# Kernel optimization log

Measured on AMD Instinct MI355X. Metric: run time of the kernel, lower is better.

Reference implementation:

```python
import jax, jax.numpy as jnp
import numpy as np
from jax import lax

NPOINT = 1024   # number of FPS centroids (init kwarg npoint)
NSAMPLE = 32    # neighbors per group (init kwarg nsample); radius is unused in the source
B, N, D = 8, 4096, 64


def setup_inputs() -> dict:
    key = jax.random.key(0)
    k1, k2, k3 = jax.random.split(key, 3)
    xyz = jax.random.normal(k1, (B, 3, N), dtype=jnp.float32)
    points = jax.random.normal(k2, (B, D, N), dtype=jnp.float32)
    farthest_init = jax.random.randint(k3, (B,), 0, N)
    return {"xyz": xyz, "points": points, "farthest_init": farthest_init}


def _fps(x, farthest_init, npoint):
    # x: [B,N,3] -> centroid indices [B,npoint]. Sequential argmax/min-update, like the torch loop.
    b, n, _ = x.shape
    bidx = jnp.arange(b)

    def step(carry, _):
        dist, far = carry                      # dist: [B,N], far: [B]
        centroid = x[bidx, far]                # [B,3]
        d = jnp.sum((x - centroid[:, None, :]) ** 2, -1)
        dist = jnp.minimum(dist, d)            # == masked update dist[mask]=d[mask]
        return (dist, jnp.argmax(dist, -1)), far

    init = (jnp.full((b, n), 1e10, dtype=x.dtype), farthest_init)
    _, cent = lax.scan(step, init, None, length=npoint)
    return cent.T                              # [B,npoint]


def _forward(xyz, points, farthest_init):
    x = xyz.transpose(0, 2, 1)                 # [B,N,3]
    p = points.transpose(0, 2, 1)              # [B,N,D]
    b = x.shape[0]
    bidx = jnp.arange(b)

    # FPS indices are non-differentiable (long tensor in torch) -> stop_gradient
    fps_idx = _fps(lax.stop_gradient(x), farthest_init, NPOINT)   # [B,S]
    new_xyz = x[bidx[:, None], fps_idx]        # [B,S,3]

    # pairwise squared distances [B,S,N] (same expansion as square_distance)
    sq = (jnp.sum(new_xyz ** 2, -1)[:, :, None]
          + jnp.sum(x ** 2, -1)[:, None, :]
          - 2.0 * jnp.einsum('bsc,bnc->bsn', new_xyz, x))
    # source sorts and takes first nsample == nsample smallest distances
    _, idx = lax.top_k(-lax.stop_gradient(sq), NSAMPLE)           # [B,S,K]

    g_xyz = x[bidx[:, None, None], idx]        # [B,S,K,3]
    g_pts = p[bidx[:, None, None], idx]        # [B,S,K,D]
    new_points = jnp.concatenate([g_xyz, g_pts], -1)              # [B,S,K,3+D]

    # permute(0,3,2,1) then max over dim 2 == max over K then transpose
    feat = jnp.max(new_points, axis=2).transpose(0, 2, 1)         # [B,3+D,S]
    return new_xyz.transpose(0, 2, 1), feat                       # [B,3,S], [B,3+D,S]


def reference(xyz, points, farthest_init):
    return _forward(xyz, points, farthest_init)
```

## Files before the change

kernel.cpp:

```cpp
#include <hip/hip_runtime.h>

#define BB 8
#define NN 4096
#define DD 64
#define SS 1024
#define KK 32
#define GINF 1e30f

typedef float f32x2 __attribute__((ext_vector_type(2)));

__device__ __forceinline__ float fmulrn(float a, float b){ return __fmul_rn(a,b); }
__device__ __forceinline__ float faddrn(float a, float b){ return __fadd_rn(a,b); }
__device__ __forceinline__ float fsubrn(float a, float b){ return __fsub_rn(a,b); }

__device__ __forceinline__ f32x2 pk_add(f32x2 a, f32x2 b){
  f32x2 d; asm("v_pk_add_f32 %0, %1, %2" : "=v"(d) : "v"(a), "v"(b)); return d;
}
__device__ __forceinline__ f32x2 pk_mul(f32x2 a, f32x2 b){
  f32x2 d; asm("v_pk_mul_f32 %0, %1, %2" : "=v"(d) : "v"(a), "v"(b)); return d;
}

template<int CTRL>
__device__ __forceinline__ float dpp_fmax(float v){
  int o = __builtin_amdgcn_update_dpp(0, __float_as_int(v), CTRL, 0xf, 0xf, true);
  return fmaxf(v, __int_as_float(o));
}

__device__ __forceinline__ float fneg_exact(float c){
  return __int_as_float(__float_as_int(c) ^ 0x80000000);
}

__global__ __launch_bounds__(256) void sqx_kernel(const float* __restrict__ xyz,
                                                  float* __restrict__ sqx){
  int i = blockIdx.x * 256 + threadIdx.x;
  int b = i >> 12, n = i & (NN - 1);
  const float* xb = xyz + b * 3 * NN;
  float x = xb[n], y = xb[NN + n], z = xb[2 * NN + n];
  sqx[i] = faddrn(faddrn(fmulrn(x, x), fmulrn(y, y)), fmulrn(z, z));
}

__global__ __launch_bounds__(256) void fps_kernel(const float* __restrict__ xyz,
                                                  const int* __restrict__ finit,
                                                  int* __restrict__ fps_idx){
  __shared__ float4 sc[2][4];
  __shared__ int    sn[2][4];
  int b = blockIdx.x, tid = threadIdx.x;
  int lane = tid & 63, w = tid >> 6;
  const float* xb = xyz + b * 3 * NN;
  f32x2 px2[8], py2[8], pz2[8], dist2[8];
  int nbase = tid << 4;
  #pragma unroll
  for (int p = 0; p < 8; ++p){
    px2[p] = ((const f32x2*)(xb + nbase))[p];
    py2[p] = ((const f32x2*)(xb + NN + nbase))[p];
    pz2[p] = ((const f32x2*)(xb + 2 * NN + nbase))[p];
    dist2[p] = (f32x2){1e10f, 1e10f};
  }
  int far = finit[b];
  float cx = xb[far], cy = xb[NN + far], cz = xb[2 * NN + far];
  if (tid == 0) fps_idx[b * SS] = far;

  for (int it = 0; it < SS - 1; ++it){
    f32x2 c2x = (f32x2){fneg_exact(cx), fneg_exact(cx)};
    f32x2 c2y = (f32x2){fneg_exact(cy), fneg_exact(cy)};
    f32x2 c2z = (f32x2){fneg_exact(cz), fneg_exact(cz)};
    float lmx = 0.0f, lmy = 0.0f;
    #pragma unroll
    for (int p = 0; p < 8; ++p){
      f32x2 tx = pk_add(px2[p], c2x);
      f32x2 ty = pk_add(py2[p], c2y);
      f32x2 tz = pk_add(pz2[p], c2z);
      f32x2 d2 = pk_add(pk_add(pk_mul(tx, tx), pk_mul(ty, ty)), pk_mul(tz, tz));
      dist2[p].x = fminf(dist2[p].x, d2.x);
      dist2[p].y = fminf(dist2[p].y, d2.y);
      lmx = fmaxf(lmx, dist2[p].x);
      lmy = fmaxf(lmy, dist2[p].y);
    }
    float lm = fmaxf(lmx, lmy);
    float v = lm;
    v = dpp_fmax<0x111>(v);
    v = dpp_fmax<0x112>(v);
    v = dpp_fmax<0x114>(v);
    v = dpp_fmax<0x118>(v);
    v = dpp_fmax<0x142>(v);
    v = dpp_fmax<0x143>(v);
    float maxv = __int_as_float(__builtin_amdgcn_readlane(__float_as_int(v), 63));
    int locA = -1, locB = -1;
    float axv = 0.f, ayv = 0.f, azv = 0.f, bxv = 0.f, byv = 0.f, bzv = 0.f;
    #pragma unroll
    for (int j = 15; j >= 8; --j){
      int p = j >> 1;
      float dv = (j & 1) ? dist2[p].y : dist2[p].x;
      if (dv == maxv){
        locB = j;
        bxv = (j & 1) ? px2[p].y : px2[p].x;
        byv = (j & 1) ? py2[p].y : py2[p].x;
        bzv = (j & 1) ? pz2[p].y : pz2[p].x;
      }
    }
    #pragma unroll
    for (int j = 7; j >= 0; --j){
      int p = j >> 1;
      float dv = (j & 1) ? dist2[p].y : dist2[p].x;
      if (dv == maxv){
        locA = j;
        axv = (j & 1) ? px2[p].y : px2[p].x;
        ayv = (j & 1) ? py2[p].y : py2[p].x;
        azv = (j & 1) ? pz2[p].y : pz2[p].x;
      }
    }
    bool fa = locA >= 0;
    int   loc = fa ? locA : locB;
    float scx = fa ? axv : bxv;
    float scy = fa ? ayv : byv;
    float scz = fa ? azv : bzv;
    unsigned long long bal = __ballot(loc >= 0);
    int fl = __ffsll(bal) - 1;
    int par = it & 1;
    if (lane == fl){
      sc[par][w] = make_float4(scx, scy, scz, maxv);
      sn[par][w] = nbase + loc;
    }
    __syncthreads();
    float4 s0 = sc[par][0]; int n0 = sn[par][0];
    #pragma unroll
    for (int q = 1; q < 4; ++q){
      float4 sq_ = sc[par][q]; int nq = sn[par][q];
      if (sq_.w > s0.w){ s0 = sq_; n0 = nq; }
    }
    cx = s0.x; cy = s0.y; cz = s0.z;
    if (tid == 0) fps_idx[b * SS + it + 1] = n0;
  }
}

__global__ __launch_bounds__(256) void knn_kernel(const float* __restrict__ xyz,
                                                  const float* __restrict__ points,
                                                  const float* __restrict__ sqx,
                                                  const int* __restrict__ fps_idx,
                                                  float* __restrict__ out){
  __shared__ int nbr[4][KK];
  int tid = threadIdx.x;
  int lane = tid & 63, wslot = tid >> 6;
  int gw = blockIdx.x * 4 + wslot;
  int b = gw >> 10, cs = gw & 1023;
  const float* xb = xyz + b * 3 * NN;
  const float* sb = sqx + b * NN;
  int c0 = fps_idx[b * SS + cs];
  float cx = xb[c0], cy = xb[NN + c0], cz = xb[2 * NN + c0];
  float sqc = sb[c0];

  float d[64];
  #pragma unroll
  for (int k = 0; k < 64; ++k){
    int n = (k << 6) | lane;
    float xn = xb[n], yn = xb[NN + n], zn = xb[2 * NN + n], sn = sb[n];
    float dot = faddrn(faddrn(fmulrn(cx, xn), fmulrn(cy, yn)), fmulrn(cz, zn));
    d[k] = fsubrn(faddrn(sqc, sn), fmulrn(2.0f, dot));
  }

  float gv[8]; int gn[8];
  #pragma unroll
  for (int j = 0; j < 8; ++j){
    float nv = GINF; int nn2 = 0x40000000;
    #pragma unroll
    for (int t = 0; t < 8; ++t){
      int k = j * 8 + t; int n = (k << 6) | lane;
      if (d[k] < nv){ nv = d[k]; nn2 = n; }
    }
    gv[j] = nv; gn[j] = nn2;
  }

  float lv = -GINF; int ln = -1;
  for (int r = 0; r < KK; ++r){
    float bv = gv[0]; int bn = gn[0];
    #pragma unroll
    for (int j = 1; j < 8; ++j){ if (gv[j] < bv){ bv = gv[j]; bn = gn[j]; } }
    #pragma unroll
    for (int m = 1; m < 64; m <<= 1){
      float ov = __shfl_xor(bv, m);
      int   on = __shfl_xor(bn, m);
      if (ov < bv || (ov == bv && on < bn)){ bv = ov; bn = on; }
    }
    if (lane == 0) nbr[wslot][r] = bn;
    lv = bv; ln = bn;
    int jsel = __builtin_amdgcn_readfirstlane(bn >> 9);
    #define RECOMP(J) if (jsel == (J)) { float nv = GINF; int nn2 = 0x40000000; \
      _Pragma("unroll") \
      for (int t = 0; t < 8; ++t){ int k = (J) * 8 + t; int n = (k << 6) | lane; \
        bool pass = (d[k] > lv) || (d[k] == lv && n > ln); \
        if (pass && d[k] < nv){ nv = d[k]; nn2 = n; } } \
      gv[(J)] = nv; gn[(J)] = nn2; }
    RECOMP(0) RECOMP(1) RECOMP(2) RECOMP(3)
    RECOMP(4) RECOMP(5) RECOMP(6) RECOMP(7)
    #undef RECOMP
  }
  __syncthreads();

  const float* pb = points + b * DD * NN;
  float fm = -GINF, xm = -GINF, ym = -GINF, zm = -GINF;
  #pragma unroll 8
  for (int j = 0; j < KK; ++j){
    int nj = nbr[wslot][j];
    fm = fmaxf(fm, pb[lane * NN + nj]);
    xm = fmaxf(xm, xb[nj]);
    ym = fmaxf(ym, xb[NN + nj]);
    zm = fmaxf(zm, xb[2 * NN + nj]);
  }
  float* out1 = out + BB * 3 * SS;
  float* o1b  = out1 + b * 67 * SS;
  o1b[(3 + lane) * SS + cs] = fm;
  if (lane == 0){
    o1b[cs] = xm; o1b[SS + cs] = ym; o1b[2 * SS + cs] = zm;
    float* o0b = out + b * 3 * SS;
    o0b[cs] = cx; o0b[SS + cs] = cy; o0b[2 * SS + cs] = cz;
  }
}

extern "C" void kernel_launch(void* const* d_in, const int* in_sizes, int n_in,
                              void* d_out, int out_size, void* d_ws, size_t ws_size,
                              hipStream_t stream){
  const float* xyz    = (const float*)d_in[0];
  const float* points = (const float*)d_in[1];
  const int*   finit  = (const int*)d_in[2];
  float* out = (float*)d_out;
  int*   fps_idx = (int*)d_ws;
  float* sqx     = (float*)((char*)d_ws + BB * SS * sizeof(int));

  hipLaunchKernelGGL(sqx_kernel, dim3(BB * NN / 256), dim3(256), 0, stream, xyz, sqx);
  hipLaunchKernelGGL(fps_kernel, dim3(BB), dim3(256), 0, stream, xyz, finit, fps_idx);
  hipLaunchKernelGGL(knn_kernel, dim3(BB * SS / 4), dim3(256), 0, stream,
                     xyz, points, sqx, fps_idx, out);
}
```

Before: 1.258 ms.

## Process two batches per FPS block to interleave independent reduction chains

The FPS kernel now handles two batch elements per 256-thread block and interleaves their distance updates, argmax searches, wave reductions and barriers. The aim is to hide the latency of the serial per-iteration reduction and barrier chain by giving each wave two independent dependency chains, and to halve the barrier count per batch. The local argmax location search now runs before the wave reduction, compared against the lane-local max instead of the wave max. The cost is doubled register use per thread and only four blocks instead of eight, so the work is spread over fewer CUs.

```diff
diff --git a/kernel.cpp b/kernel.cpp
--- a/kernel.cpp
+++ b/kernel.cpp
@@ -24,6 +24,17 @@
 __device__ __forceinline__ float dpp_fmax(float v){
   int o = __builtin_amdgcn_update_dpp(0, __float_as_int(v), CTRL, 0xf, 0xf, true);
   return fmaxf(v, __int_as_float(o));
+}
+
+__device__ __forceinline__ float wave_max_dpp(float lm){
+  float v = lm;
+  v = dpp_fmax<0x111>(v);
+  v = dpp_fmax<0x112>(v);
+  v = dpp_fmax<0x114>(v);
+  v = dpp_fmax<0x118>(v);
+  v = dpp_fmax<0x142>(v);
+  v = dpp_fmax<0x143>(v);
+  return __int_as_float(__builtin_amdgcn_readlane(__float_as_int(v), 63));
 }
 
 __device__ __forceinline__ float fneg_exact(float c){
@@ -42,94 +53,142 @@
 __global__ __launch_bounds__(256) void fps_kernel(const float* __restrict__ xyz,
                                                   const int* __restrict__ finit,
                                                   int* __restrict__ fps_idx){
-  __shared__ float4 sc[2][4];
-  __shared__ int    sn[2][4];
-  int b = blockIdx.x, tid = threadIdx.x;
+  __shared__ float4 scA[2][4], scB[2][4];
+  __shared__ int    snA[2][4], snB[2][4];
+  int blk = blockIdx.x, tid = threadIdx.x;
   int lane = tid & 63, w = tid >> 6;
-  const float* xb = xyz + b * 3 * NN;
-  f32x2 px2[8], py2[8], pz2[8], dist2[8];
+  int bA = blk * 2, bB = blk * 2 + 1;
+  const float* xA = xyz + bA * 3 * NN;
+  const float* xB = xyz + bB * 3 * NN;
   int nbase = tid << 4;
+
+  f32x2 pxA[8], pyA[8], pzA[8], ddA[8];
+  f32x2 pxB[8], pyB[8], pzB[8], ddB[8];
   #pragma unroll
   for (int p = 0; p < 8; ++p){
-    px2[p] = ((const f32x2*)(xb + nbase))[p];
-    py2[p] = ((const f32x2*)(xb + NN + nbase))[p];
-    pz2[p] = ((const f32x2*)(xb + 2 * NN + nbase))[p];
-    dist2[p] = (f32x2){1e10f, 1e10f};
-  }
-  int far = finit[b];
-  float cx = xb[far], cy = xb[NN + far], cz = xb[2 * NN + far];
-  if (tid == 0) fps_idx[b * SS] = far;
+    pxA[p] = ((const f32x2*)(xA + nbase))[p];
+    pyA[p] = ((const f32x2*)(xA + NN + nbase))[p];
+    pzA[p] = ((const f32x2*)(xA + 2 * NN + nbase))[p];
+    pxB[p] = ((const f32x2*)(xB + nbase))[p];
+    pyB[p] = ((const f32x2*)(xB + NN + nbase))[p];
+    pzB[p] = ((const f32x2*)(xB + 2 * NN + nbase))[p];
+    ddA[p] = (f32x2){1e10f, 1e10f};
+    ddB[p] = (f32x2){1e10f, 1e10f};
+  }
+  int farA = finit[bA], farB = finit[bB];
+  float cxA = xA[farA], cyA = xA[NN + farA], czA = xA[2 * NN + farA];
+  float cxB = xB[farB], cyB = xB[NN + farB], czB = xB[2 * NN + farB];
+  if (tid == 0){ fps_idx[bA * SS] = farA; fps_idx[bB * SS] = farB; }
 
   for (int it = 0; it < SS - 1; ++it){
-    f32x2 c2x = (f32x2){fneg_exact(cx), fneg_exact(cx)};
-    f32x2 c2y = (f32x2){fneg_exact(cy), fneg_exact(cy)};
-    f32x2 c2z = (f32x2){fneg_exact(cz), fneg_exact(cz)};
-    float lmx = 0.0f, lmy = 0.0f;
+    f32x2 ncxA = {fneg_exact(cxA), fneg_exact(cxA)};
+    f32x2 ncyA = {fneg_exact(cyA), fneg_exact(cyA)};
+    f32x2 nczA = {fneg_exact(czA), fneg_exact(czA)};
+    f32x2 ncxB = {fneg_exact(cxB), fneg_exact(cxB)};
+    f32x2 ncyB = {fneg_exact(cyB), fneg_exact(cyB)};
+    f32x2 nczB = {fneg_exact(czB), fneg_exact(czB)};
+    float lmxA = 0.f, lmyA = 0.f, lmxB = 0.f, lmyB = 0.f;
     #pragma unroll
     for (int p = 0; p < 8; ++p){
-      f32x2 tx = pk_add(px2[p], c2x);
-      f32x2 ty = pk_add(py2[p], c2y);
-      f32x2 tz = pk_add(pz2[p], c2z);
+      f32x2 tx = pk_add(pxA[p], ncxA);
+      f32x2 ty = pk_add(pyA[p], ncyA);
+      f32x2 tz = pk_add(pzA[p], nczA);
       f32x2 d2 = pk_add(pk_add(pk_mul(tx, tx), pk_mul(ty, ty)), pk_mul(tz, tz));
-      dist2[p].x = fminf(dist2[p].x, d2.x);
-      dist2[p].y = fminf(dist2[p].y, d2.y);
-      lmx = fmaxf(lmx, dist2[p].x);
-      lmy = fmaxf(lmy, dist2[p].y);
-    }
-    float lm = fmaxf(lmx, lmy);
-    float v = lm;
-    v = dpp_fmax<0x111>(v);
-    v = dpp_fmax<0x112>(v);
-    v = dpp_fmax<0x114>(v);
-    v = dpp_fmax<0x118>(v);
-    v = dpp_fmax<0x142>(v);
-    v = dpp_fmax<0x143>(v);
-    float maxv = __int_as_float(__builtin_amdgcn_readlane(__float_as_int(v), 63));
-    int locA = -1, locB = -1;
-    float axv = 0.f, ayv = 0.f, azv = 0.f, bxv = 0.f, byv = 0.f, bzv = 0.f;
+      ddA[p].x = fminf(ddA[p].x, d2.x);
+      ddA[p].y = fminf(ddA[p].y, d2.y);
+      lmxA = fmaxf(lmxA, ddA[p].x);
+      lmyA = fmaxf(lmyA, ddA[p].y);
+    }
+    #pragma unroll
+    for (int p = 0; p < 8; ++p){
+      f32x2 tx = pk_add(pxB[p], ncxB);
+      f32x2 ty = pk_add(pyB[p], ncyB);
+      f32x2 tz = pk_add(pzB[p], nczB);
+      f32x2 d2 = pk_add(pk_add(pk_mul(tx, tx), pk_mul(ty, ty)), pk_mul(tz, tz));
+      ddB[p].x = fminf(ddB[p].x, d2.x);
+      ddB[p].y = fminf(ddB[p].y, d2.y);
+      lmxB = fmaxf(lmxB, ddB[p].x);
+      lmyB = fmaxf(lmyB, ddB[p].y);
+    }
+    float lmA = fmaxf(lmxA, lmyA);
+    float lmB = fmaxf(lmxB, lmyB);
+
+    int locA1 = -1, locA2 = -1, locB1 = -1, locB2 = -1;
+    float a1x=0.f,a1y=0.f,a1z=0.f, a2x=0.f,a2y=0.f,a2z=0.f;
+    float b1x=0.f,b1y=0.f,b1z=0.f, b2x=0.f,b2y=0.f,b2z=0.f;
     #pragma unroll
     for (int j = 15; j >= 8; --j){
       int p = j >> 1;
-      float dv = (j & 1) ? dist2[p].y : dist2[p].x;
-      if (dv == maxv){
-        locB = j;
-        bxv = (j & 1) ? px2[p].y : px2[p].x;
-        byv = (j & 1) ? py2[p].y : py2[p].x;
-        bzv = (j & 1) ? pz2[p].y : pz2[p].x;
-      }
+      float dv = (j & 1) ? ddA[p].y : ddA[p].x;
+      if (dv == lmA){ locA2 = j;
+        a2x = (j & 1) ? pxA[p].y : pxA[p].x;
+        a2y = (j & 1) ? pyA[p].y : pyA[p].x;
+        a2z = (j & 1) ? pzA[p].y : pzA[p].x; }
     }
     #pragma unroll
     for (int j = 7; j >= 0; --j){
       int p = j >> 1;
-      float dv = (j & 1) ? dist2[p].y : dist2[p].x;
-      if (dv == maxv){
-        locA = j;
-        axv = (j & 1) ? px2[p].y : px2[p].x;
-        ayv = (j & 1) ? py2[p].y : py2[p].x;
-        azv = (j & 1) ? pz2[p].y : pz2[p].x;
-      }
-    }
-    bool fa = locA >= 0;
-    int   loc = fa ? locA : locB;
-    float scx = fa ? axv : bxv;
-    float scy = fa ? ayv : byv;
-    float scz = fa ? azv : bzv;
-    unsigned long long bal = __ballot(loc >= 0);
-    int fl = __ffsll(bal) - 1;
+      float dv = (j & 1) ? ddA[p].y : ddA[p].x;
+      if (dv == lmA){ locA1 = j;
+        a1x = (j & 1) ? pxA[p].y : pxA[p].x;
+        a1y = (j & 1) ? pyA[p].y : pyA[p].x;
+        a1z = (j & 1) ? pzA[p].y : pzA[p].x; }
+    }
+    #pragma unroll
+    for (int j = 15; j >= 8; --j){
+      int p = j >> 1;
+      float dv = (j & 1) ? ddB[p].y : ddB[p].x;
+      if (dv == lmB){ locB2 = j;
+        b2x = (j & 1) ? pxB[p].y : pxB[p].x;
+        b2y = (j & 1) ? pyB[p].y : pyB[p].x;
+        b2z = (j & 1) ? pzB[p].y : pzB[p].x; }
+    }
+    #pragma unroll
+    for (int j = 7; j >= 0; --j){
+      int p = j >> 1;
+      float dv = (j & 1) ? ddB[p].y : ddB[p].x;
+      if (dv == lmB){ locB1 = j;
+        b1x = (j & 1) ? pxB[p].y : pxB[p].x;
+        b1y = (j & 1) ? pyB[p].y : pyB[p].x;
+        b1z = (j & 1) ? pzB[p].y : pzB[p].x; }
+    }
+    bool faA = locA1 >= 0;
+    int   jlocA = faA ? locA1 : locA2;
+    float sAx = faA ? a1x : a2x, sAy = faA ? a1y : a2y, sAz = faA ? a1z : a2z;
+    bool faB = locB1 >= 0;
+    int   jlocB = faB ? locB1 : locB2;
+    float sBx = faB ? b1x : b2x, sBy = faB ? b1y : b2y, sBz = faB ? b1z : b2z;
+
+    float maxvA = wave_max_dpp(lmA);
+    float maxvB = wave_max_dpp(lmB);
+
+    unsigned long long balA = __ballot(lmA == maxvA);
+    unsigned long long balB = __ballot(lmB == maxvB);
+    int flA = __ffsll(balA) - 1;
+    int flB = __ffsll(balB) - 1;
     int par = it & 1;
-    if (lane == fl){
-      sc[par][w] = make_float4(scx, scy, scz, maxv);
-      sn[par][w] = nbase + loc;
-    }
+    if (lane == flA){ scA[par][w] = make_float4(sAx, sAy, sAz, maxvA); snA[par][w] = nbase + jlocA; }
+    if (lane == flB){ scB[par][w] = make_float4(sBx, sBy, sBz, maxvB); snB[par][w] = nbase + jlocB; }
     __syncthreads();
-    float4 s0 = sc[par][0]; int n0 = sn[par][0];
+
+    float4 s0 = scA[par][0]; int n0 = snA[par][0];
     #pragma unroll
     for (int q = 1; q < 4; ++q){
-      float4 sq_ = sc[par][q]; int nq = sn[par][q];
+      float4 sq_ = scA[par][q]; int nq = snA[par][q];
       if (sq_.w > s0.w){ s0 = sq_; n0 = nq; }
     }
-    cx = s0.x; cy = s0.y; cz = s0.z;
-    if (tid == 0) fps_idx[b * SS + it + 1] = n0;
+    cxA = s0.x; cyA = s0.y; czA = s0.z;
+    float4 t0 = scB[par][0]; int m0 = snB[par][0];
+    #pragma unroll
+    for (int q = 1; q < 4; ++q){
+      float4 tq_ = scB[par][q]; int mq = snB[par][q];
+      if (tq_.w > t0.w){ t0 = tq_; m0 = mq; }
+    }
+    cxB = t0.x; cyB = t0.y; czB = t0.z;
+    if (tid == 0){
+      fps_idx[bA * SS + it + 1] = n0;
+      fps_idx[bB * SS + it + 1] = m0;
+    }
   }
 }
 
@@ -227,7 +286,7 @@
   float* sqx     = (float*)((char*)d_ws + BB * SS * sizeof(int));
 
   hipLaunchKernelGGL(sqx_kernel, dim3(BB * NN / 256), dim3(256), 0, stream, xyz, sqx);
-  hipLaunchKernelGGL(fps_kernel, dim3(BB), dim3(256), 0, stream, xyz, finit, fps_idx);
+  hipLaunchKernelGGL(fps_kernel, dim3(BB / 2), dim3(256), 0, stream, xyz, finit, fps_idx);
   hipLaunchKernelGGL(knn_kernel, dim3(BB * SS / 4), dim3(256), 0, stream,
                      xyz, points, sqx, fps_idx, out);
 }
```

Result: slower. 2.566 ms (+104.0%).
